# Performance work log

Measured on AMD Instinct MI355X. Metric: run time of the kernel, lower is better.

## Reference

```python
import jax, jax.numpy as jnp
import numpy as np
from jax import lax

TAU = 20.0
DT = 1.0
V_TH = 1.0
V_RESET = 0.0


def lif_spike(x):
    # Heaviside spike (surrogate gradient only matters for backward)
    return (x > 0).astype(x.dtype)


def setup_inputs() -> dict:
    key = jax.random.key(0)
    k1, k2, k3 = jax.random.split(key, 3)
    T, B, IN, OUT = 100, 256, 1024, 1024
    input_spikes = jax.random.uniform(k1, (T, B, IN), dtype=jnp.float32)
    # nn.Linear default init: U(-1/sqrt(in), 1/sqrt(in)) scale; randn*0.03 is fine for a numeric baseline
    W = jax.random.normal(k2, (OUT, IN), dtype=jnp.float32) * (1.0 / np.sqrt(IN))
    b = jax.random.normal(k3, (OUT,), dtype=jnp.float32) * 0.01
    return {"input_spikes": input_spikes, "W": W, "b": b}


def reference(input_spikes, W, b):
    T, B, _ = input_spikes.shape
    OUT = W.shape[0]
    # Precompute all input currents with one big GEMM: [T,B,out]
    I_all = jnp.einsum('tbi,oi->tbo', input_spikes, W) + b

    def step(v, I):
        v = v + (-v / TAU + I) * DT          # leaky integration
        s = lif_spike(v - V_TH)              # threshold
        v = jnp.where(s > 0, V_RESET, v)     # reset on spike
        return v, s

    v0 = jnp.zeros((B, OUT), dtype=input_spikes.dtype)
    _, spikes = lax.scan(step, v0, I_all)
    return spikes  # [T, B, out]
```

## Files before the change

### kernel.cpp

```cpp
#include <hip/hip_runtime.h>


constexpr int kT   = 100;
constexpr int kB   = 256;
constexpr int kIn  = 1024;
constexpr int kOut = 1024;
constexpr int kM   = kT * kB;

constexpr int BM = 128;
constexpr int BN = 128;
constexpr int BK = 32;

__global__ __launch_bounds__(256, 3)
void gemm_f32(const float* __restrict__ A,
              const float* __restrict__ W,
              const float* __restrict__ bias,
              float* __restrict__ I)
{
    __shared__ float As[BK * BM];
    __shared__ float Ws[BK * BN];

    const int tid = threadIdx.x;
    const int m0  = blockIdx.y * BM;
    const int n0  = blockIdx.x * BN;

    const int tc = tid & 15;
    const int tr = tid >> 4;

    const int sr  = tid >> 1;
    const int sc0 = (tid & 1) * 16;

    float4 la[4], lw[4];
#pragma unroll
    for (int i = 0; i < 4; ++i) {
        la[i] = *reinterpret_cast<const float4*>(&A[(size_t)(m0 + sr) * kIn + sc0 + i * 4]);
        lw[i] = *reinterpret_cast<const float4*>(&W[(size_t)(n0 + sr) * kIn + sc0 + i * 4]);
    }

    float acc[8][8];
#pragma unroll
    for (int j = 0; j < 8; ++j)
#pragma unroll
        for (int l = 0; l < 8; ++l) acc[j][l] = 0.0f;

    for (int k0 = 0; k0 < kIn; k0 += BK) {
        __syncthreads();

#pragma unroll
        for (int i = 0; i < 4; ++i) {
            const float* lap = reinterpret_cast<const float*>(&la[i]);
            const float* lwp = reinterpret_cast<const float*>(&lw[i]);
#pragma unroll
            for (int kk = 0; kk < 4; ++kk) {
                const int k = sc0 + i * 4 + kk;
                As[k * BM + sr] = lap[kk];
                Ws[k * BN + sr] = lwp[kk];
            }
        }

        __syncthreads();

        if (k0 + BK < kIn) {
#pragma unroll
            for (int i = 0; i < 4; ++i) {
                la[i] = *reinterpret_cast<const float4*>(&A[(size_t)(m0 + sr) * kIn + (k0 + BK) + sc0 + i * 4]);
                lw[i] = *reinterpret_cast<const float4*>(&W[(size_t)(n0 + sr) * kIn + (k0 + BK) + sc0 + i * 4]);
            }
        }

#pragma unroll 2
        for (int k = 0; k < BK; ++k) {
            const float4 a0 = *reinterpret_cast<const float4*>(&As[k * BM + tr * 8]);
            const float4 a1 = *reinterpret_cast<const float4*>(&As[k * BM + tr * 8 + 4]);
            const float4 w0 = *reinterpret_cast<const float4*>(&Ws[k * BN + tc * 8]);
            const float4 w1 = *reinterpret_cast<const float4*>(&Ws[k * BN + tc * 8 + 4]);
            const float a[8] = {a0.x, a0.y, a0.z, a0.w, a1.x, a1.y, a1.z, a1.w};
            const float w[8] = {w0.x, w0.y, w0.z, w0.w, w1.x, w1.y, w1.z, w1.w};
#pragma unroll
            for (int j = 0; j < 8; ++j)
#pragma unroll
                for (int l = 0; l < 8; ++l)
                    acc[j][l] = fmaf(a[j], w[l], acc[j][l]);
        }
    }

#pragma unroll
    for (int j = 0; j < 8; ++j) {
        const int m = m0 + tr * 8 + j;
#pragma unroll
        for (int h = 0; h < 2; ++h) {
            const int n = n0 + tc * 8 + h * 4;
            float4 o4;
            o4.x = acc[j][h * 4 + 0] + bias[n + 0];
            o4.y = acc[j][h * 4 + 1] + bias[n + 1];
            o4.z = acc[j][h * 4 + 2] + bias[n + 2];
            o4.w = acc[j][h * 4 + 3] + bias[n + 3];
            *reinterpret_cast<float4*>(&I[(size_t)m * kOut + n]) = o4;
        }
    }
}

__global__ __launch_bounds__(256)
void lif_scan_f32(const float* Iin, float* out)
{
    const int idx4 = (blockIdx.x * blockDim.x + threadIdx.x) * 4;
    if (idx4 >= kB * kOut) return;

    float v0 = 0.0f, v1 = 0.0f, v2 = 0.0f, v3 = 0.0f;
    for (int t = 0; t < kT; ++t) {
        const size_t off = (size_t)t * (kB * kOut) + idx4;
        const float4 Iv = *reinterpret_cast<const float4*>(&Iin[off]);
        float4 s4;

        { const float t1 = v0 / 20.0f; const float u = Iv.x - t1; v0 = v0 + u;
          const bool s = (v0 > 1.0f); s4.x = s ? 1.0f : 0.0f; if (s) v0 = 0.0f; }
        { const float t1 = v1 / 20.0f; const float u = Iv.y - t1; v1 = v1 + u;
          const bool s = (v1 > 1.0f); s4.y = s ? 1.0f : 0.0f; if (s) v1 = 0.0f; }
        { const float t1 = v2 / 20.0f; const float u = Iv.z - t1; v2 = v2 + u;
          const bool s = (v2 > 1.0f); s4.z = s ? 1.0f : 0.0f; if (s) v2 = 0.0f; }
        { const float t1 = v3 / 20.0f; const float u = Iv.w - t1; v3 = v3 + u;
          const bool s = (v3 > 1.0f); s4.w = s ? 1.0f : 0.0f; if (s) v3 = 0.0f; }

        *reinterpret_cast<float4*>(&out[off]) = s4;
    }
}

extern "C" void kernel_launch(void* const* d_in, const int* in_sizes, int n_in,
                              void* d_out, int out_size, void* d_ws, size_t ws_size,
                              hipStream_t stream) {
    const float* spikes = (const float*)d_in[0];
    const float* W      = (const float*)d_in[1];
    const float* bias   = (const float*)d_in[2];
    float* out = (float*)d_out;

    const size_t iBytes = (size_t)kM * kOut * sizeof(float);
    dim3 grid(kOut / BN, kM / BM);

    float* Ibuf = (ws_size >= iBytes && d_ws != nullptr) ? (float*)d_ws : out;
    gemm_f32<<<grid, 256, 0, stream>>>(spikes, W, bias, Ibuf);
    lif_scan_f32<<<(kB * kOut) / (256 * 4), 256, 0, stream>>>(Ibuf, out);
}
```

Baseline: 671.1 us.

## Enlarge GEMM tile to 256x128 with 16x8 microtile and swizzled W smem

Doubles the GEMM block tile in M to 256 and gives each thread a 16x8 accumulator microtile, which raises arithmetic intensity per shared-memory load. A row-per-thread A staging pattern replaces the old one, W columns are XOR-swizzled in shared memory to reduce bank conflicts, and the bias is loaded once as float4. The cost is much higher register pressure (128 accumulators), with occupancy lowered to 2 blocks per CU and a risk of spills.

```diff
diff --git a/kernel.cpp b/kernel.cpp
--- a/kernel.cpp
+++ b/kernel.cpp
@@ -7,11 +7,11 @@
 constexpr int kOut = 1024;
 constexpr int kM   = kT * kB;
 
-constexpr int BM = 128;
+constexpr int BM = 256;
 constexpr int BN = 128;
 constexpr int BK = 32;
 
-__global__ __launch_bounds__(256, 3)
+__global__ __launch_bounds__(256, 2)
 void gemm_f32(const float* __restrict__ A,
               const float* __restrict__ W,
               const float* __restrict__ bias,
@@ -27,19 +27,26 @@
     const int tc = tid & 15;
     const int tr = tid >> 4;
 
-    const int sr  = tid >> 1;
-    const int sc0 = (tid & 1) * 16;
+    const int pw0 = (((2 * tc)     ) ^ ((2 * tc)     >> 2)) * 4;
+    const int pw1 = (((2 * tc + 1) ) ^ ((2 * tc + 1) >> 2)) * 4;
 
-    float4 la[4], lw[4];
+    const float* Arow = A + (size_t)(m0 + tid) * kIn;
+    const int    wn   = tid >> 1;
+    const int    wk0  = (tid & 1) * 16;
+    const float* Wrow = W + (size_t)(n0 + wn) * kIn + wk0;
+    const int    wslot = ((wn >> 2) ^ (wn >> 4)) * 4 + (wn & 3);
+
+    float4 la[8], lw[4];
 #pragma unroll
-    for (int i = 0; i < 4; ++i) {
-        la[i] = *reinterpret_cast<const float4*>(&A[(size_t)(m0 + sr) * kIn + sc0 + i * 4]);
-        lw[i] = *reinterpret_cast<const float4*>(&W[(size_t)(n0 + sr) * kIn + sc0 + i * 4]);
-    }
+    for (int i = 0; i < 8; ++i)
+        la[i] = *reinterpret_cast<const float4*>(Arow + i * 4);
+#pragma unroll
+    for (int i = 0; i < 4; ++i)
+        lw[i] = *reinterpret_cast<const float4*>(Wrow + i * 4);
 
-    float acc[8][8];
+    float acc[16][8];
 #pragma unroll
-    for (int j = 0; j < 8; ++j)
+    for (int j = 0; j < 16; ++j)
 #pragma unroll
         for (int l = 0; l < 8; ++l) acc[j][l] = 0.0f;
 
@@ -47,55 +54,65 @@
         __syncthreads();
 
 #pragma unroll
+        for (int i = 0; i < 8; ++i) {
+            const float* p = reinterpret_cast<const float*>(&la[i]);
+#pragma unroll
+            for (int j = 0; j < 4; ++j)
+                As[(i * 4 + j) * BM + tid] = p[j];
+        }
+#pragma unroll
         for (int i = 0; i < 4; ++i) {
-            const float* lap = reinterpret_cast<const float*>(&la[i]);
-            const float* lwp = reinterpret_cast<const float*>(&lw[i]);
+            const float* p = reinterpret_cast<const float*>(&lw[i]);
 #pragma unroll
-            for (int kk = 0; kk < 4; ++kk) {
-                const int k = sc0 + i * 4 + kk;
-                As[k * BM + sr] = lap[kk];
-                Ws[k * BN + sr] = lwp[kk];
-            }
+            for (int j = 0; j < 4; ++j)
+                Ws[(wk0 + i * 4 + j) * BN + wslot] = p[j];
         }
 
         __syncthreads();
 
         if (k0 + BK < kIn) {
+            const int kn = k0 + BK;
 #pragma unroll
-            for (int i = 0; i < 4; ++i) {
-                la[i] = *reinterpret_cast<const float4*>(&A[(size_t)(m0 + sr) * kIn + (k0 + BK) + sc0 + i * 4]);
-                lw[i] = *reinterpret_cast<const float4*>(&W[(size_t)(n0 + sr) * kIn + (k0 + BK) + sc0 + i * 4]);
-            }
+            for (int i = 0; i < 8; ++i)
+                la[i] = *reinterpret_cast<const float4*>(Arow + kn + i * 4);
+#pragma unroll
+            for (int i = 0; i < 4; ++i)
+                lw[i] = *reinterpret_cast<const float4*>(Wrow + kn + i * 4);
         }
 
-#pragma unroll 2
+#pragma unroll 4
         for (int k = 0; k < BK; ++k) {
-            const float4 a0 = *reinterpret_cast<const float4*>(&As[k * BM + tr * 8]);
-            const float4 a1 = *reinterpret_cast<const float4*>(&As[k * BM + tr * 8 + 4]);
-            const float4 w0 = *reinterpret_cast<const float4*>(&Ws[k * BN + tc * 8]);
-            const float4 w1 = *reinterpret_cast<const float4*>(&Ws[k * BN + tc * 8 + 4]);
-            const float a[8] = {a0.x, a0.y, a0.z, a0.w, a1.x, a1.y, a1.z, a1.w};
-            const float w[8] = {w0.x, w0.y, w0.z, w0.w, w1.x, w1.y, w1.z, w1.w};
+            const float4 a0 = *reinterpret_cast<const float4*>(&As[k * BM + tr * 16 +  0]);
+            const float4 a1 = *reinterpret_cast<const float4*>(&As[k * BM + tr * 16 +  4]);
+            const float4 a2 = *reinterpret_cast<const float4*>(&As[k * BM + tr * 16 +  8]);
+            const float4 a3 = *reinterpret_cast<const float4*>(&As[k * BM + tr * 16 + 12]);
+            const float4 w0 = *reinterpret_cast<const float4*>(&Ws[k * BN + pw0]);
+            const float4 w1 = *reinterpret_cast<const float4*>(&Ws[k * BN + pw1]);
+            const float a[16] = {a0.x, a0.y, a0.z, a0.w, a1.x, a1.y, a1.z, a1.w,
+                                 a2.x, a2.y, a2.z, a2.w, a3.x, a3.y, a3.z, a3.w};
+            const float w[8]  = {w0.x, w0.y, w0.z, w0.w, w1.x, w1.y, w1.z, w1.w};
 #pragma unroll
-            for (int j = 0; j < 8; ++j)
+            for (int j = 0; j < 16; ++j)
 #pragma unroll
                 for (int l = 0; l < 8; ++l)
                     acc[j][l] = fmaf(a[j], w[l], acc[j][l]);
         }
     }
 
+    const float4 b0 = *reinterpret_cast<const float4*>(&bias[n0 + tc * 8]);
+    const float4 b1 = *reinterpret_cast<const float4*>(&bias[n0 + tc * 8 + 4]);
+    const float bb[8] = {b0.x, b0.y, b0.z, b0.w, b1.x, b1.y, b1.z, b1.w};
 #pragma unroll
-    for (int j = 0; j < 8; ++j) {
-        const int m = m0 + tr * 8 + j;
+    for (int j = 0; j < 16; ++j) {
+        const int m = m0 + tr * 16 + j;
 #pragma unroll
         for (int h = 0; h < 2; ++h) {
-            const int n = n0 + tc * 8 + h * 4;
             float4 o4;
-            o4.x = acc[j][h * 4 + 0] + bias[n + 0];
-            o4.y = acc[j][h * 4 + 1] + bias[n + 1];
-            o4.z = acc[j][h * 4 + 2] + bias[n + 2];
-            o4.w = acc[j][h * 4 + 3] + bias[n + 3];
-            *reinterpret_cast<float4*>(&I[(size_t)m * kOut + n]) = o4;
+            o4.x = acc[j][h * 4 + 0] + bb[h * 4 + 0];
+            o4.y = acc[j][h * 4 + 1] + bb[h * 4 + 1];
+            o4.z = acc[j][h * 4 + 2] + bb[h * 4 + 2];
+            o4.w = acc[j][h * 4 + 3] + bb[h * 4 + 3];
+            *reinterpret_cast<float4*>(&I[(size_t)m * kOut + n0 + tc * 8 + h * 4]) = o4;
         }
     }
 }
```

After: 843.3 us. 25.7% more time.
